# Optimization experiments

Measured on AMD Instinct MI355X. Metric: run time of the kernel, lower is better.

## Reference

```python
import jax, jax.numpy as jnp
import numpy as np

N_NODES = 100000
N_EDGES = 800000
NODE_DIM = 64
EDGE_DIM = 64
GEO_DIM = 8
GEO_OUT = 32
COND_DIM = 512
N_GRAPHS = 64
JOIN_DIM = EDGE_DIM + GEO_OUT  # 96


def setup_inputs() -> dict:
    key = jax.random.key(0)
    ks = jax.random.split(key, 10)
    return {
        "node_feats": jax.random.normal(ks[0], (N_NODES, NODE_DIM), jnp.float32),
        "edge_index": jax.random.randint(ks[1], (2, N_EDGES), 0, N_NODES, jnp.int64),
        "e_geo": jax.random.normal(ks[2], (N_EDGES, GEO_DIM), jnp.float32),
        "cond": jax.random.normal(ks[3], (N_GRAPHS, COND_DIM), jnp.float32),
        "edge_batch_ids": jax.random.randint(ks[4], (N_EDGES,), 0, N_GRAPHS, jnp.int64),
        "Wn": jax.random.normal(ks[5], (NODE_DIM, EDGE_DIM), jnp.float32) / np.sqrt(NODE_DIM),
        "bn": jnp.zeros((EDGE_DIM,), jnp.float32),
        "Wg": jax.random.normal(ks[6], (GEO_DIM, GEO_OUT), jnp.float32) / np.sqrt(GEO_DIM),
        "bg": jnp.zeros((GEO_OUT,), jnp.float32),
        "Wc": jax.random.normal(ks[7], (COND_DIM, 2 * EDGE_DIM), jnp.float32) / np.sqrt(COND_DIM),
        "bc": jnp.zeros((2 * EDGE_DIM,), jnp.float32),
        "Wx": jax.random.normal(ks[8], (JOIN_DIM, EDGE_DIM), jnp.float32) / np.sqrt(JOIN_DIM),
    }


def reference(node_feats, edge_index, e_geo, cond, edge_batch_ids,
              Wn, bn, Wg, bg, Wc, bc, Wx):
    # n_proj: project node features  [N, node_dim] -> [N, edge_dim]
    n_proj = node_feats @ Wn + bn
    # combine_node_attr 'mul': gather to edge endpoints and multiply  [E, edge_dim]
    src = n_proj[edge_index[0]]
    dst = n_proj[edge_index[1]]
    n_join = src * dst
    # e_geo_linear: [E, geo_dim] -> [E, geo_out]
    eg = e_geo @ Wg + bg
    # join features [E, edge_dim + geo_out]
    join = jnp.concatenate([n_join, eg], axis=-1)
    # FilmFusion: cond_proj -> gamma/beta per graph, gather to edges
    gb = cond @ Wc + bc                      # [B, 2*edge_dim]
    gamma, beta = jnp.split(gb, 2, axis=-1)
    gamma = gamma + 1.0
    gamma_e = gamma[edge_batch_ids]          # [E, edge_dim]
    beta_e = beta[edge_batch_ids]
    # x_linear (bias=False), FiLM modulation, relu
    x = join @ Wx
    return jax.nn.relu(x * gamma_e + beta_e)
```

## Files before the change

### kernel.cpp

```cpp
#include <hip/hip_runtime.h>
#include <hip/hip_bf16.h>

#define N_NODES   100000
#define N_EDGES   800000
#define NODE_DIM  64
#define EDGE_DIM  64
#define GEO_DIM   8
#define GEO_OUT   32
#define COND_DIM  512
#define N_GRAPHS  64

typedef short  bf8   __attribute__((ext_vector_type(8)));
typedef float  f32x4 __attribute__((ext_vector_type(4)));
typedef unsigned short u16x8 __attribute__((ext_vector_type(8)));

__device__ __forceinline__ float b2f(unsigned short u) {
    return __uint_as_float(((unsigned)u) << 16);
}
__device__ __forceinline__ short f2b(float f) {
    unsigned u = __float_as_uint(f);
    u = (u + 0x7FFFu + ((u >> 16) & 1u)) >> 16;
    return (short)u;
}
__device__ __forceinline__ unsigned f2b2(float lo, float hi) {
    __hip_bfloat162 h = __float22bfloat162_rn(make_float2(lo, hi));
    union { __hip_bfloat162 h; unsigned u; } cv;
    cv.h = h;
    return cv.u;
}
__device__ __forceinline__ float rdlane(float v, int l) {
    return __int_as_float(__builtin_amdgcn_readlane(__float_as_int(v), l));
}

__global__ __launch_bounds__(128) void prep_kernel(
        const float* __restrict__ cond, const float* __restrict__ Wc,
        const float* __restrict__ bc,   const float* __restrict__ Wg,
        const float* __restrict__ bg,   const float* __restrict__ Wx,
        float* __restrict__ gamma, float* __restrict__ beta2,
        unsigned short* __restrict__ Bfrag) {
    int t = threadIdx.x;
    int g = blockIdx.x;
    if (g < N_GRAPHS) {
        __shared__ float condl[COND_DIM];
        __shared__ float gbl[128];
        for (int i = t; i < COND_DIM; i += 128) condl[i] = cond[g * COND_DIM + i];
        __syncthreads();
        float acc = bc[t];
        #pragma unroll 8
        for (int k = 0; k < COND_DIM; ++k) acc += condl[k] * Wc[k * 128 + t];
        gbl[t] = acc;
        __syncthreads();
        if (t < 64) {
            float gam = gbl[t] + 1.0f;
            float bet = gbl[64 + t];
            float cv = 0.0f;
            #pragma unroll
            for (int i = 0; i < GEO_OUT; ++i) cv += bg[i] * Wx[(64 + i) * 64 + t];
            gamma[g * 64 + t] = gam;
            beta2[g * 64 + t] = bet + cv * gam;
        }
    } else {
        for (int idx = t; idx < 6144; idx += 128) {
            int j    = idx & 7;
            int lane = (idx >> 3) & 63;
            int ct   = idx >> 9;
            int c    = ct >> 2, tt = ct & 3;
            int k = c * 32 + ((lane >> 4) & 3) * 8 + j;
            int n = tt * 16 + (lane & 15);
            float val;
            if (k < 64) {
                val = Wx[k * 64 + n];
            } else if (k < 72) {
                float s = 0.f;
                #pragma unroll
                for (int i = 0; i < GEO_OUT; ++i)
                    s += Wg[(k - 64) * GEO_OUT + i] * Wx[(64 + i) * 64 + n];
                val = s;
            } else {
                val = 0.f;
            }
            Bfrag[idx] = (unsigned short)f2b(val);
        }
    }
}

__global__ __launch_bounds__(256) void nproj_kernel(
        const float* __restrict__ nf, const float* __restrict__ Wn,
        const float* __restrict__ bn, unsigned short* __restrict__ nprojb) {
    int lane = threadIdx.x & 63;
    int wid    = (blockIdx.x * blockDim.x + threadIdx.x) >> 6;
    int nwaves = (gridDim.x * blockDim.x) >> 6;
    float wcol[64];
    #pragma unroll
    for (int k = 0; k < 64; ++k) wcol[k] = Wn[k * 64 + lane];
    float bnl = bn[lane];
    for (int node = wid; node < N_NODES; node += nwaves) {
        float v = nf[(size_t)node * 64 + lane];
        float a0 = 0.f, a1 = 0.f, a2 = 0.f, a3 = bnl;
        #pragma unroll
        for (int k = 0; k < 64; k += 4) {
            a0 = fmaf(rdlane(v, k    ), wcol[k    ], a0);
            a1 = fmaf(rdlane(v, k + 1), wcol[k + 1], a1);
            a2 = fmaf(rdlane(v, k + 2), wcol[k + 2], a2);
            a3 = fmaf(rdlane(v, k + 3), wcol[k + 3], a3);
        }
        nprojb[(size_t)node * 64 + lane] = (unsigned short)f2b((a0 + a1) + (a2 + a3));
    }
}

__global__ __launch_bounds__(256) void edge_kernel(
        const unsigned short* __restrict__ nprojb,
        const int*   __restrict__ eidx,
        const float* __restrict__ egeo,
        const int*   __restrict__ ebatch,
        const unsigned short* __restrict__ Bfrag,
        const float* __restrict__ gamma,
        const float* __restrict__ beta2,
        float* __restrict__ out) {
    int lane = threadIdx.x & 63;
    int q  = lane >> 4;
    int mm = lane & 15;
    int wv = threadIdx.x >> 6;
    int wid    = (blockIdx.x * blockDim.x + threadIdx.x) >> 6;
    int nwaves = (gridDim.x * blockDim.x) >> 6;

    __shared__ float ldsT[4][16 * 64];
    float* tileb = ldsT[wv];

    bf8 bfrag[3][4];
    #pragma unroll
    for (int c = 0; c < 3; ++c)
        #pragma unroll
        for (int t = 0; t < 4; ++t)
            bfrag[c][t] = *(const bf8*)(Bfrag + (size_t)((c * 4 + t) * 64 + lane) * 8);

    const int NTILES = N_EDGES / 16;
    for (int tile = wid; tile < NTILES; tile += nwaves) {
        int e0 = tile * 16;
        int e  = e0 + mm;
        int s = __builtin_nontemporal_load(eidx + e);
        int d = __builtin_nontemporal_load(eidx + N_EDGES + e);
        int bq[4];
        #pragma unroll
        for (int c = 0; c < 4; ++c)
            bq[c] = __builtin_nontemporal_load(ebatch + e0 + c * 4 + q);

        const u16x8* ps = (const u16x8*)(nprojb + (size_t)s * 64 + q * 8);
        const u16x8* pd = (const u16x8*)(nprojb + (size_t)d * 64 + q * 8);
        u16x8 s0 = ps[0], s1 = ps[4];
        u16x8 d0 = pd[0], d1 = pd[4];

        union { bf8 v; unsigned u[4]; } A0, A1, A2;
        #pragma unroll
        for (int j = 0; j < 8; j += 2) {
            A0.u[j >> 1] = f2b2(b2f(s0[j]) * b2f(d0[j]), b2f(s0[j + 1]) * b2f(d0[j + 1]));
            A1.u[j >> 1] = f2b2(b2f(s1[j]) * b2f(d1[j]), b2f(s1[j + 1]) * b2f(d1[j + 1]));
            A2.u[j >> 1] = 0u;
        }
        if (q == 0) {
            f32x4 g0 = __builtin_nontemporal_load((const f32x4*)(egeo + (size_t)e * 8));
            f32x4 g1 = __builtin_nontemporal_load((const f32x4*)(egeo + (size_t)e * 8 + 4));
            A2.u[0] = f2b2(g0[0], g0[1]);
            A2.u[1] = f2b2(g0[2], g0[3]);
            A2.u[2] = f2b2(g1[0], g1[1]);
            A2.u[3] = f2b2(g1[2], g1[3]);
        }

        f32x4 acc[4];
        #pragma unroll
        for (int t = 0; t < 4; ++t) {
            f32x4 c = {0.f, 0.f, 0.f, 0.f};
            c = __builtin_amdgcn_mfma_f32_16x16x32_bf16(A0.v, bfrag[0][t], c, 0, 0, 0);
            c = __builtin_amdgcn_mfma_f32_16x16x32_bf16(A1.v, bfrag[1][t], c, 0, 0, 0);
            c = __builtin_amdgcn_mfma_f32_16x16x32_bf16(A2.v, bfrag[2][t], c, 0, 0, 0);
            acc[t] = c;
        }

        #pragma unroll
        for (int t = 0; t < 4; ++t)
            #pragma unroll
            for (int i = 0; i < 4; ++i)
                tileb[(q * 4 + i) * 64 + t * 16 + mm] = acc[t][i];
        asm volatile("s_waitcnt lgkmcnt(0)" ::: "memory");

        #pragma unroll
        for (int c = 0; c < 4; ++c) {
            int row = c * 4 + q;
            int b   = bq[c];
            f32x4 v  = *(const f32x4*)&tileb[row * 64 + mm * 4];
            f32x4 gm = *(const f32x4*)(gamma + b * 64 + mm * 4);
            f32x4 bt = *(const f32x4*)(beta2 + b * 64 + mm * 4);
            f32x4 r;
            #pragma unroll
            for (int i = 0; i < 4; ++i) {
                float x = fmaf(v[i], gm[i], bt[i]);
                r[i] = x > 0.f ? x : 0.f;
            }
            __builtin_nontemporal_store(r, (f32x4*)(out + (size_t)e0 * 64 + c * 256 + lane * 4));
        }
    }
}

extern "C" void kernel_launch(void* const* d_in, const int* in_sizes, int n_in,
                              void* d_out, int out_size, void* d_ws, size_t ws_size,
                              hipStream_t stream) {
    const float* node_feats = (const float*)d_in[0];
    const int*   edge_index = (const int*)  d_in[1];
    const float* e_geo      = (const float*)d_in[2];
    const float* cond       = (const float*)d_in[3];
    const int*   ebatch     = (const int*)  d_in[4];
    const float* Wn         = (const float*)d_in[5];
    const float* bn         = (const float*)d_in[6];
    const float* Wg         = (const float*)d_in[7];
    const float* bg         = (const float*)d_in[8];
    const float* Wc         = (const float*)d_in[9];
    const float* bc         = (const float*)d_in[10];
    const float* Wx         = (const float*)d_in[11];
    float* out = (float*)d_out;

    char* ws = (char*)d_ws;
    float*          gamma  = (float*)(ws);
    float*          beta2  = (float*)(ws + 16384);
    unsigned short* Bfrag  = (unsigned short*)(ws + 32768);
    unsigned short* nprojb = (unsigned short*)(ws + 49152);

    hipLaunchKernelGGL(prep_kernel, dim3(65), dim3(128), 0, stream,
                       cond, Wc, bc, Wg, bg, Wx, gamma, beta2, Bfrag);
    hipLaunchKernelGGL(nproj_kernel, dim3(3125), dim3(256), 0, stream,
                       node_feats, Wn, bn, nprojb);
    hipLaunchKernelGGL(edge_kernel, dim3(6250), dim3(256), 0, stream,
                       nprojb, edge_index, e_geo, ebatch, Bfrag, gamma, beta2, out);
}
```

Before: 373.0 us.

## Swap MFMA operands to drop LDS transpose and merge prep with nproj

The edge kernel swaps the MFMA A/B operands so each lane's accumulator holds four consecutive output columns of its own edge. The epilogue can then apply FiLM and store directly from registers, with no LDS round-trip and its waitcnt. Each lane now loads one batch id, but the gamma/beta reads and output stores become per-edge rows with 16-byte strided writes instead of fully contiguous wave stores. The prep and node-projection kernels are also fused into one launch to save one kernel launch.

```diff
diff --git a/kernel.cpp b/kernel.cpp
--- a/kernel.cpp
+++ b/kernel.cpp
@@ -32,23 +32,27 @@
     return __int_as_float(__builtin_amdgcn_readlane(__float_as_int(v), l));
 }
 
-__global__ __launch_bounds__(128) void prep_kernel(
+__global__ __launch_bounds__(256) void prep_nproj_kernel(
         const float* __restrict__ cond, const float* __restrict__ Wc,
         const float* __restrict__ bc,   const float* __restrict__ Wg,
         const float* __restrict__ bg,   const float* __restrict__ Wx,
+        const float* __restrict__ nf,   const float* __restrict__ Wn,
+        const float* __restrict__ bn,
         float* __restrict__ gamma, float* __restrict__ beta2,
-        unsigned short* __restrict__ Bfrag) {
+        unsigned short* __restrict__ Bfrag, unsigned short* __restrict__ nprojb) {
     int t = threadIdx.x;
     int g = blockIdx.x;
     if (g < N_GRAPHS) {
         __shared__ float condl[COND_DIM];
         __shared__ float gbl[128];
-        for (int i = t; i < COND_DIM; i += 128) condl[i] = cond[g * COND_DIM + i];
+        for (int i = t; i < COND_DIM; i += 256) condl[i] = cond[g * COND_DIM + i];
         __syncthreads();
-        float acc = bc[t];
-        #pragma unroll 8
-        for (int k = 0; k < COND_DIM; ++k) acc += condl[k] * Wc[k * 128 + t];
-        gbl[t] = acc;
+        if (t < 128) {
+            float acc = bc[t];
+            #pragma unroll 8
+            for (int k = 0; k < COND_DIM; ++k) acc += condl[k] * Wc[k * 128 + t];
+            gbl[t] = acc;
+        }
         __syncthreads();
         if (t < 64) {
             float gam = gbl[t] + 1.0f;
@@ -59,8 +63,8 @@
             gamma[g * 64 + t] = gam;
             beta2[g * 64 + t] = bet + cv * gam;
         }
-    } else {
-        for (int idx = t; idx < 6144; idx += 128) {
+    } else if (g == N_GRAPHS) {
+        for (int idx = t; idx < 6144; idx += 256) {
             int j    = idx & 7;
             int lane = (idx >> 3) & 63;
             int ct   = idx >> 9;
@@ -81,30 +85,26 @@
             }
             Bfrag[idx] = (unsigned short)f2b(val);
         }
-    }
-}
-
-__global__ __launch_bounds__(256) void nproj_kernel(
-        const float* __restrict__ nf, const float* __restrict__ Wn,
-        const float* __restrict__ bn, unsigned short* __restrict__ nprojb) {
-    int lane = threadIdx.x & 63;
-    int wid    = (blockIdx.x * blockDim.x + threadIdx.x) >> 6;
-    int nwaves = (gridDim.x * blockDim.x) >> 6;
-    float wcol[64];
-    #pragma unroll
-    for (int k = 0; k < 64; ++k) wcol[k] = Wn[k * 64 + lane];
-    float bnl = bn[lane];
-    for (int node = wid; node < N_NODES; node += nwaves) {
-        float v = nf[(size_t)node * 64 + lane];
-        float a0 = 0.f, a1 = 0.f, a2 = 0.f, a3 = bnl;
-        #pragma unroll
-        for (int k = 0; k < 64; k += 4) {
-            a0 = fmaf(rdlane(v, k    ), wcol[k    ], a0);
-            a1 = fmaf(rdlane(v, k + 1), wcol[k + 1], a1);
-            a2 = fmaf(rdlane(v, k + 2), wcol[k + 2], a2);
-            a3 = fmaf(rdlane(v, k + 3), wcol[k + 3], a3);
-        }
-        nprojb[(size_t)node * 64 + lane] = (unsigned short)f2b((a0 + a1) + (a2 + a3));
+    } else {
+        int lane = t & 63;
+        int wid    = (((g - N_GRAPHS - 1) << 8) + t) >> 6;
+        const int nwaves = (3125 * 256) >> 6;
+        float wcol[64];
+        #pragma unroll
+        for (int k = 0; k < 64; ++k) wcol[k] = Wn[k * 64 + lane];
+        float bnl = bn[lane];
+        for (int node = wid; node < N_NODES; node += nwaves) {
+            float v = nf[(size_t)node * 64 + lane];
+            float a0 = 0.f, a1 = 0.f, a2 = 0.f, a3 = bnl;
+            #pragma unroll
+            for (int k = 0; k < 64; k += 4) {
+                a0 = fmaf(rdlane(v, k    ), wcol[k    ], a0);
+                a1 = fmaf(rdlane(v, k + 1), wcol[k + 1], a1);
+                a2 = fmaf(rdlane(v, k + 2), wcol[k + 2], a2);
+                a3 = fmaf(rdlane(v, k + 3), wcol[k + 3], a3);
+            }
+            nprojb[(size_t)node * 64 + lane] = (unsigned short)f2b((a0 + a1) + (a2 + a3));
+        }
     }
 }
 
@@ -120,12 +120,8 @@
     int lane = threadIdx.x & 63;
     int q  = lane >> 4;
     int mm = lane & 15;
-    int wv = threadIdx.x >> 6;
     int wid    = (blockIdx.x * blockDim.x + threadIdx.x) >> 6;
     int nwaves = (gridDim.x * blockDim.x) >> 6;
-
-    __shared__ float ldsT[4][16 * 64];
-    float* tileb = ldsT[wv];
 
     bf8 bfrag[3][4];
     #pragma unroll
@@ -140,10 +136,7 @@
         int e  = e0 + mm;
         int s = __builtin_nontemporal_load(eidx + e);
         int d = __builtin_nontemporal_load(eidx + N_EDGES + e);
-        int bq[4];
-        #pragma unroll
-        for (int c = 0; c < 4; ++c)
-            bq[c] = __builtin_nontemporal_load(ebatch + e0 + c * 4 + q);
+        int b = __builtin_nontemporal_load(ebatch + e);
 
         const u16x8* ps = (const u16x8*)(nprojb + (size_t)s * 64 + q * 8);
         const u16x8* pd = (const u16x8*)(nprojb + (size_t)d * 64 + q * 8);
@@ -166,37 +159,26 @@
             A2.u[3] = f2b2(g1[2], g1[3]);
         }
 
-        f32x4 acc[4];
+        const float* gp = gamma + b * 64 + q * 4;
+        const float* bp = beta2 + b * 64 + q * 4;
+        float* op = out + (size_t)e * 64 + q * 4;
+
         #pragma unroll
         for (int t = 0; t < 4; ++t) {
             f32x4 c = {0.f, 0.f, 0.f, 0.f};
-            c = __builtin_amdgcn_mfma_f32_16x16x32_bf16(A0.v, bfrag[0][t], c, 0, 0, 0);
-            c = __builtin_amdgcn_mfma_f32_16x16x32_bf16(A1.v, bfrag[1][t], c, 0, 0, 0);
-            c = __builtin_amdgcn_mfma_f32_16x16x32_bf16(A2.v, bfrag[2][t], c, 0, 0, 0);
-            acc[t] = c;
-        }
-
-        #pragma unroll
-        for (int t = 0; t < 4; ++t)
-            #pragma unroll
-            for (int i = 0; i < 4; ++i)
-                tileb[(q * 4 + i) * 64 + t * 16 + mm] = acc[t][i];
-        asm volatile("s_waitcnt lgkmcnt(0)" ::: "memory");
-
-        #pragma unroll
-        for (int c = 0; c < 4; ++c) {
-            int row = c * 4 + q;
-            int b   = bq[c];
-            f32x4 v  = *(const f32x4*)&tileb[row * 64 + mm * 4];
-            f32x4 gm = *(const f32x4*)(gamma + b * 64 + mm * 4);
-            f32x4 bt = *(const f32x4*)(beta2 + b * 64 + mm * 4);
+            c = __builtin_amdgcn_mfma_f32_16x16x32_bf16(bfrag[0][t], A0.v, c, 0, 0, 0);
+            c = __builtin_amdgcn_mfma_f32_16x16x32_bf16(bfrag[1][t], A1.v, c, 0, 0, 0);
+            c = __builtin_amdgcn_mfma_f32_16x16x32_bf16(bfrag[2][t], A2.v, c, 0, 0, 0);
+
+            f32x4 gm = *(const f32x4*)(gp + t * 16);
+            f32x4 bt = *(const f32x4*)(bp + t * 16);
             f32x4 r;
             #pragma unroll
             for (int i = 0; i < 4; ++i) {
-                float x = fmaf(v[i], gm[i], bt[i]);
+                float x = fmaf(c[i], gm[i], bt[i]);
                 r[i] = x > 0.f ? x : 0.f;
             }
-            __builtin_nontemporal_store(r, (f32x4*)(out + (size_t)e0 * 64 + c * 256 + lane * 4));
+            __builtin_nontemporal_store(r, (f32x4*)(op + t * 16));
         }
     }
 }
@@ -224,10 +206,9 @@
     unsigned short* Bfrag  = (unsigned short*)(ws + 32768);
     unsigned short* nprojb = (unsigned short*)(ws + 49152);
 
-    hipLaunchKernelGGL(prep_kernel, dim3(65), dim3(128), 0, stream,
-                       cond, Wc, bc, Wg, bg, Wx, gamma, beta2, Bfrag);
-    hipLaunchKernelGGL(nproj_kernel, dim3(3125), dim3(256), 0, stream,
-                       node_feats, Wn, bn, nprojb);
+    hipLaunchKernelGGL(prep_nproj_kernel, dim3(65 + 3125), dim3(256), 0, stream,
+                       cond, Wc, bc, Wg, bg, Wx, node_feats, Wn, bn,
+                       gamma, beta2, Bfrag, nprojb);
     hipLaunchKernelGGL(edge_kernel, dim3(6250), dim3(256), 0, stream,
                        nprojb, edge_index, e_geo, ebatch, Bfrag, gamma, beta2, out);
 }
```

After: 394.7 us. 5.8% more time.
